# Kernel tuning notes

Measured on AMD Instinct MI355X. Metric: run time of the kernel, lower is better.

The kernel has to match this reference:

```python
import jax, jax.numpy as jnp
import numpy as np

B, S, D, H = 4, 2048, 1024, 16
DK = D // H

def setup_inputs() -> dict:
    key = jax.random.key(0)
    ks = jax.random.split(key, 13)
    std = 1.0 / np.sqrt(D)
    inp = {
        'query': jax.random.normal(ks[0], (B, S, D), jnp.float32),
        'key':   jax.random.normal(ks[1], (B, S, D), jnp.float32),
        'value': jax.random.normal(ks[2], (B, S, D), jnp.float32),
        'mask':  jax.random.randint(ks[3], (B, 1, S), 0, 2, jnp.int32),
        'Wq': jax.random.normal(ks[4], (D, D), jnp.float32) * std,
        'bq': jnp.zeros((D,), jnp.float32),
        'Wk': jax.random.normal(ks[5], (D, D), jnp.float32) * std,
        'bk': jnp.zeros((D,), jnp.float32),
        'Wv': jax.random.normal(ks[6], (D, D), jnp.float32) * std,
        'bv': jnp.zeros((D,), jnp.float32),
        'Wo': jax.random.normal(ks[7], (D, D), jnp.float32) * std,
        'bo': jnp.zeros((D,), jnp.float32),
    }
    return inp

def reference(query, key, value, mask, Wq, bq, Wk, bk, Wv, bv, Wo, bo):
    # QKV projections (torch Linear: x @ W.T + b), reshape to [B,H,S,DK]
    def proj(x, W, b):
        y = x @ W.T + b
        return y.reshape(B, S, H, DK).transpose(0, 2, 1, 3)
    q = proj(query, Wq, bq)
    k = proj(key, Wk, bk)
    v = proj(value, Wv, bv)
    scores = jnp.einsum('bhqd,bhkd->bhqk', q, k) / jnp.sqrt(jnp.float32(DK))
    # mask [B,1,S] -> unsqueeze head dim -> [B,1,1,S], broadcast over h,q
    m = mask[:, None, :, :]  # [B,1,1,S]
    scores = jnp.where(m == 0, jnp.float32(-1e9), scores)
    p = jax.nn.softmax(scores, axis=-1)  # dropout omitted (eval mode)
    x = jnp.einsum('bhqk,bhkd->bhqd', p, v)
    x = x.transpose(0, 2, 1, 3).reshape(B, S, D)
    return x @ Wo.T + bo
```

## Files before the change

kernel.cpp:

```cpp
#include <hip/hip_runtime.h>

typedef unsigned short u16;
typedef __bf16 bf16x8 __attribute__((ext_vector_type(8)));
typedef float f32x4 __attribute__((ext_vector_type(4)));
typedef u16 u16x8 __attribute__((ext_vector_type(8)));
typedef u16 u16x4 __attribute__((ext_vector_type(4)));

typedef __attribute__((address_space(1))) const unsigned char gc_u8;
typedef __attribute__((address_space(3))) unsigned char lds_u8;

__device__ inline void gload16(const void* g, void* l) {
    __builtin_amdgcn_global_load_lds((gc_u8*)g, (lds_u8*)l, 16, 0, 0);
}
__device__ inline u16 f2bf(float f) {
    union { __bf16 h; u16 u; } c; c.h = (__bf16)f; return c.u;
}
__device__ inline float bf2f(u16 u) {
    union { u16 u[2]; float f; } c; c.u[0] = 0; c.u[1] = u; return c.f;
}
__device__ inline void hard_barrier() {
    __builtin_amdgcn_sched_barrier(0);
    __builtin_amdgcn_s_barrier();
    __builtin_amdgcn_sched_barrier(0);
}
#define WAIT_LGKM0() asm volatile("s_waitcnt lgkmcnt(0)" ::: "memory")
#define WAIT_VMCNT(n) asm volatile("s_waitcnt vmcnt(" #n ")" ::: "memory")

__global__ __launch_bounds__(256) void cvt4(const float* __restrict__ s0,
                                            const float* __restrict__ s1,
                                            const float* __restrict__ s2,
                                            const float* __restrict__ s3,
                                            u16* __restrict__ d0, u16* __restrict__ d1,
                                            u16* __restrict__ d2, u16* __restrict__ d3,
                                            int n) {
    const int y = blockIdx.y;
    const float* src = (y == 0) ? s0 : (y == 1) ? s1 : (y == 2) ? s2 : s3;
    u16* dst = (y == 0) ? d0 : (y == 1) ? d1 : (y == 2) ? d2 : d3;
    int i = (blockIdx.x * 256 + threadIdx.x) * 4;
    if (i < n) {
        float4 f = *reinterpret_cast<const float4*>(src + i);
        u16x4 u = { f2bf(f.x), f2bf(f.y), f2bf(f.z), f2bf(f.w) };
        *reinterpret_cast<u16x4*>(dst + i) = u;
    }
}

__global__ __launch_bounds__(256) void gemm_qkv(const float* __restrict__ Aq,
                                                const float* __restrict__ Ak,
                                                const float* __restrict__ Av,
                                                const u16* __restrict__ Bq,
                                                const u16* __restrict__ Bk,
                                                const u16* __restrict__ Bv,
                                                const float* __restrict__ bq,
                                                const float* __restrict__ bk,
                                                const float* __restrict__ bv,
                                                u16* __restrict__ Cq,
                                                u16* __restrict__ Ck,
                                                u16* __restrict__ Cvp,
                                                int M, int N, int K) {
    __shared__ __align__(16) float Asf[2][128][32];
    __shared__ __align__(16) u16 Bs[2][128][32];
    const int z = blockIdx.z;
    const float* A = (z == 0) ? Aq : (z == 1) ? Ak : Av;
    const u16* B = (z == 0) ? Bq : (z == 1) ? Bk : Bv;
    const float* bias = (z == 0) ? bq : (z == 1) ? bk : bv;
    u16* Cv = (z == 0) ? Cq : (z == 1) ? Ck : Cvp;
    const bool vmode = (z == 2);

    const int t = threadIdx.x, lane = t & 63, w = t >> 6;
    const int wr = w >> 1, wc = w & 1;
    const int l15 = lane & 15, l16 = lane >> 4;
    const int nwg = gridDim.x, ntiles = N >> 7;
    const int wg = blockIdx.x, chunk = nwg >> 3;
    const int swz = (wg & 7) * chunk + (wg >> 3);
    const int bm = (swz / ntiles) * 128, bn = (swz % ntiles) * 128;
    const int srow = w * 16 + (lane >> 2);
    const int sgr = (lane & 3) * 8;
    const int arsub = lane >> 3;
    const int agr = ((lane & 7) ^ (lane >> 3)) * 4;
    const u16* Bb = B + (size_t)bn * K;

    f32x4 acc[4][4];
#pragma unroll
    for (int i = 0; i < 4; i++)
#pragma unroll
        for (int j = 0; j < 4; j++) acc[i][j] = (f32x4){0.f, 0.f, 0.f, 0.f};

    auto stage = [&](int c, int k0) {
#pragma unroll
        for (int ch = 0; ch < 4; ch++)
            gload16(A + (size_t)(bm + ch * 32 + w * 8 + arsub) * K + k0 + agr,
                    &Asf[c][ch * 32 + w * 8][0]);
        gload16(Bb + (size_t)srow * K + k0 + sgr,        &Bs[c][w * 16][0]);
        gload16(Bb + (size_t)(64 + srow) * K + k0 + sgr, &Bs[c][64 + w * 16][0]);
    };

    stage(0, 0);
    __syncthreads();

    const int NS = K >> 5;
    for (int i = 0; i < NS; ++i) {
        const int c = i & 1;
        WAIT_LGKM0();
        hard_barrier();
        if (i + 1 < NS) {
            stage(c ^ 1, (i + 1) * 32);
            WAIT_VMCNT(6);
        } else {
            WAIT_VMCNT(0);
        }
        hard_barrier();

        const int key = l15 & 7;
        bf16x8 afr[4], bfr[4];
#pragma unroll
        for (int mi = 0; mi < 4; mi++) {
            const int rr = wr * 64 + mi * 16 + l15;
            f32x4 lo = *(const f32x4*)&Asf[c][rr][((2 * l16) ^ key) * 4];
            f32x4 hi = *(const f32x4*)&Asf[c][rr][((2 * l16 + 1) ^ key) * 4];
            bf16x8 v;
            v[0] = (__bf16)lo[0]; v[1] = (__bf16)lo[1];
            v[2] = (__bf16)lo[2]; v[3] = (__bf16)lo[3];
            v[4] = (__bf16)hi[0]; v[5] = (__bf16)hi[1];
            v[6] = (__bf16)hi[2]; v[7] = (__bf16)hi[3];
            afr[mi] = v;
        }
#pragma unroll
        for (int ni = 0; ni < 4; ni++)
            bfr[ni] = *(const bf16x8*)&Bs[c][wc * 64 + ni * 16 + l15][l16 * 8];
#pragma unroll
        for (int mi = 0; mi < 4; mi++)
#pragma unroll
            for (int ni = 0; ni < 4; ni++)
                acc[mi][ni] = __builtin_amdgcn_mfma_f32_16x16x32_bf16(
                    afr[mi], bfr[ni], acc[mi][ni], 0, 0, 0);
    }

#pragma unroll
    for (int ni = 0; ni < 4; ni++) {
        const int col = bn + wc * 64 + ni * 16 + l15;
        const float bv2 = bias[col];
#pragma unroll
        for (int mi = 0; mi < 4; mi++) {
            const int r0 = bm + wr * 64 + mi * 16 + l16 * 4;
            if (vmode) {
                const int bb = r0 >> 11, ss = r0 & 2047;
                const int hh = col >> 6, dk = col & 63;
                u16x4 pk;
#pragma unroll
                for (int r = 0; r < 4; r++) pk[r] = f2bf(acc[mi][ni][r] + bv2);
                *(u16x4*)&Cv[(((size_t)(bb * 16 + hh) * 64 + dk) << 11) + ss] = pk;
            } else {
#pragma unroll
                for (int r = 0; r < 4; r++)
                    Cv[(size_t)(r0 + r) * N + col] = f2bf(acc[mi][ni][r] + bv2);
            }
        }
    }
}

__global__ __launch_bounds__(256) void gemm_out(const u16* __restrict__ A,
                                                const u16* __restrict__ B,
                                                const float* __restrict__ bias,
                                                float* __restrict__ Cv,
                                                int M, int N, int K) {
    __shared__ __align__(16) u16 As[2][128][32];
    __shared__ __align__(16) u16 Bs[2][128][32];
    const int t = threadIdx.x, lane = t & 63, w = t >> 6;
    const int wr = w >> 1, wc = w & 1;
    const int l15 = lane & 15, l16 = lane >> 4;
    const int nwg = gridDim.x, ntiles = N >> 7;
    const int wg = blockIdx.x, chunk = nwg >> 3;
    const int swz = (wg & 7) * chunk + (wg >> 3);
    const int bm = (swz / ntiles) * 128, bn = (swz % ntiles) * 128;
    const int srow = w * 16 + (lane >> 2);
    const int sgr = (lane & 3) * 8;
    const u16* Ab = A + (size_t)bm * K;
    const u16* Bb = B + (size_t)bn * K;

    f32x4 acc[4][4];
#pragma unroll
    for (int i = 0; i < 4; i++)
#pragma unroll
        for (int j = 0; j < 4; j++) acc[i][j] = (f32x4){0.f, 0.f, 0.f, 0.f};

    auto stage = [&](int c, int k0) {
        gload16(Ab + (size_t)srow * K + k0 + sgr,        &As[c][w * 16][0]);
        gload16(Ab + (size_t)(64 + srow) * K + k0 + sgr, &As[c][64 + w * 16][0]);
        gload16(Bb + (size_t)srow * K + k0 + sgr,        &Bs[c][w * 16][0]);
        gload16(Bb + (size_t)(64 + srow) * K + k0 + sgr, &Bs[c][64 + w * 16][0]);
    };

    stage(0, 0);
    __syncthreads();

    const int NS = K >> 5;
    for (int i = 0; i < NS; ++i) {
        const int c = i & 1;
        WAIT_LGKM0();
        hard_barrier();
        if (i + 1 < NS) {
            stage(c ^ 1, (i + 1) * 32);
            WAIT_VMCNT(4);
        } else {
            WAIT_VMCNT(0);
        }
        hard_barrier();

        bf16x8 afr[4], bfr[4];
#pragma unroll
        for (int mi = 0; mi < 4; mi++)
            afr[mi] = *(const bf16x8*)&As[c][wr * 64 + mi * 16 + l15][l16 * 8];
#pragma unroll
        for (int ni = 0; ni < 4; ni++)
            bfr[ni] = *(const bf16x8*)&Bs[c][wc * 64 + ni * 16 + l15][l16 * 8];
#pragma unroll
        for (int mi = 0; mi < 4; mi++)
#pragma unroll
            for (int ni = 0; ni < 4; ni++)
                acc[mi][ni] = __builtin_amdgcn_mfma_f32_16x16x32_bf16(
                    afr[mi], bfr[ni], acc[mi][ni], 0, 0, 0);
    }

#pragma unroll
    for (int ni = 0; ni < 4; ni++) {
        const int col = bn + wc * 64 + ni * 16 + l15;
        const float bv = bias[col];
#pragma unroll
        for (int mi = 0; mi < 4; mi++) {
            const int r0 = bm + wr * 64 + mi * 16 + l16 * 4;
#pragma unroll
            for (int r = 0; r < 4; r++)
                Cv[(size_t)(r0 + r) * N + col] = acc[mi][ni][r] + bv;
        }
    }
}

__global__ __launch_bounds__(256, 2) void attn_fwd(const u16* __restrict__ Q,
                                                   const u16* __restrict__ Kg,
                                                   const u16* __restrict__ Vt,
                                                   const int* __restrict__ mask,
                                                   u16* __restrict__ O) {
    constexpr int S = 2048, D = 1024;
    __shared__ __align__(16) u16 Kl[2][2][2][64][32];
    __shared__ __align__(16) u16 Vl[2][2][2][64][32];
    __shared__ __align__(16) u16 Pl[4][16][68];
    __shared__ unsigned Mb[64];
    const int t = threadIdx.x, lane = t & 63, w = t >> 6;
    const int l15 = lane & 15, l16 = lane >> 4;
    const int wg = blockIdx.x;
    const int swz = (wg & 7) * 64 + (wg >> 3);
    const int q0 = (swz & 7) * 256, h = (swz >> 3) & 15, b = swz >> 7;
    const int qb = q0 + w * 64;
    const int srow = w * 16 + (lane >> 2);
    const int sgr = ((lane & 3) ^ ((lane >> 3) & 3)) * 8;
    const int gsw8 = (l16 ^ ((l15 >> 1) & 3)) * 8;

    const u16* Khead = Kg + (size_t)b * S * D + h * 64;
    const u16* Vthead = Vt + (size_t)(b * 16 + h) * 64 * 2048;
    const int* mrow = mask + b * S;

    auto stage = [&](int c, int kt) {
#pragma unroll
        for (int kg = 0; kg < 2; kg++) {
            const int k0 = kt + kg * 64;
            gload16(Khead + (size_t)(k0 + srow) * D + sgr,        &Kl[c][kg][0][w * 16][0]);
            gload16(Khead + (size_t)(k0 + srow) * D + 32 + sgr,   &Kl[c][kg][1][w * 16][0]);
            gload16(Vthead + (size_t)srow * 2048 + k0 + sgr,      &Vl[c][kg][0][w * 16][0]);
            gload16(Vthead + (size_t)srow * 2048 + k0 + 32 + sgr, &Vl[c][kg][1][w * 16][0]);
        }
    };

    stage(0, 0);
#pragma unroll
    for (int j = 0; j < 8; j++) {
        unsigned long long bal = __ballot(mrow[j * 256 + w * 64 + lane] != 0);
        if (lane == 0) {
            Mb[(j * 4 + w) * 2]     = (unsigned)bal;
            Mb[(j * 4 + w) * 2 + 1] = (unsigned)(bal >> 32);
        }
    }

    constexpr float QSCALE = 0.125f * 1.44269504f;
    bf16x8 aq[4][2];
#pragma unroll
    for (int qt = 0; qt < 4; qt++)
#pragma unroll
        for (int ks = 0; ks < 2; ks++) {
            const size_t qi = ((size_t)b * S + qb + qt * 16 + l15) * D +
                              h * 64 + ks * 32 + l16 * 8;
            u16x8 raw = *(const u16x8*)&Q[qi];
            bf16x8 qv;
#pragma unroll
            for (int i = 0; i < 8; i++) qv[i] = (__bf16)(bf2f(raw[i]) * QSCALE);
            aq[qt][ks] = qv;
        }

    bf16x8 ones;
#pragma unroll
    for (int i = 0; i < 8; i++) ones[i] = (__bf16)1.0f;

    f32x4 acc[4][4];
    f32x4 accl[4];
#pragma unroll
    for (int qt = 0; qt < 4; qt++) {
        accl[qt] = (f32x4){0.f, 0.f, 0.f, 0.f};
#pragma unroll
        for (int dt = 0; dt < 4; dt++) acc[qt][dt] = (f32x4){0.f, 0.f, 0.f, 0.f};
    }

    __syncthreads();

    for (int tile = 0; tile < S / 128; ++tile) {
        const int c = tile & 1;
        const int cur = tile * 128;
        WAIT_LGKM0();
        hard_barrier();
        if (tile + 1 < S / 128) {
            stage(c ^ 1, cur + 128);
            WAIT_VMCNT(8);
        } else {
            WAIT_VMCNT(0);
        }
        hard_barrier();

#pragma unroll
        for (int kg = 0; kg < 2; kg++) {
            bf16x8 kf0[4], kf1[4], vf0[4], vf1[4];
#pragma unroll
            for (int k4 = 0; k4 < 4; k4++) {
                kf0[k4] = *(const bf16x8*)&Kl[c][kg][0][k4 * 16 + l15][gsw8];
                kf1[k4] = *(const bf16x8*)&Kl[c][kg][1][k4 * 16 + l15][gsw8];
            }
#pragma unroll
            for (int dt = 0; dt < 4; dt++) {
                vf0[dt] = *(const bf16x8*)&Vl[c][kg][0][dt * 16 + l15][gsw8];
                vf1[dt] = *(const bf16x8*)&Vl[c][kg][1][dt * 16 + l15][gsw8];
            }

            const int mb0 = (cur >> 5) + kg * 2;
            const unsigned w0 = Mb[mb0], w1 = Mb[mb0 + 1];
            float madd[4][4];
#pragma unroll
            for (int k4 = 0; k4 < 4; k4++) {
                const unsigned wsel = (k4 < 2) ? w0 : w1;
                const unsigned bits = (wsel >> ((k4 & 1) * 16 + l16 * 4)) & 0xFu;
#pragma unroll
                for (int r = 0; r < 4; r++)
                    madd[k4][r] = ((bits >> r) & 1u) ? 0.f : -1.0e9f;
            }

#pragma unroll
            for (int qt = 0; qt < 4; qt++) {
#pragma unroll
                for (int k4 = 0; k4 < 4; k4++) {
                    f32x4 z = (f32x4){0.f, 0.f, 0.f, 0.f};
                    z = __builtin_amdgcn_mfma_f32_16x16x32_bf16(kf0[k4], aq[qt][0], z, 0, 0, 0);
                    z = __builtin_amdgcn_mfma_f32_16x16x32_bf16(kf1[k4], aq[qt][1], z, 0, 0, 0);
                    u16x4 pk;
#pragma unroll
                    for (int r = 0; r < 4; r++)
                        pk[r] = f2bf(__builtin_amdgcn_exp2f(z[r] + madd[k4][r]));
                    *(u16x4*)&Pl[w][l15][k4 * 16 + l16 * 4] = pk;
                }
                bf16x8 pa0 = *(const bf16x8*)&Pl[w][l15][l16 * 8];
                bf16x8 pa1 = *(const bf16x8*)&Pl[w][l15][32 + l16 * 8];
                accl[qt] = __builtin_amdgcn_mfma_f32_16x16x32_bf16(pa0, ones, accl[qt], 0, 0, 0);
                accl[qt] = __builtin_amdgcn_mfma_f32_16x16x32_bf16(pa1, ones, accl[qt], 0, 0, 0);
#pragma unroll
                for (int dt = 0; dt < 4; dt++) {
                    acc[qt][dt] = __builtin_amdgcn_mfma_f32_16x16x32_bf16(
                        pa0, vf0[dt], acc[qt][dt], 0, 0, 0);
                    acc[qt][dt] = __builtin_amdgcn_mfma_f32_16x16x32_bf16(
                        pa1, vf1[dt], acc[qt][dt], 0, 0, 0);
                }
            }
        }
    }

#pragma unroll
    for (int qt = 0; qt < 4; qt++) {
        f32x4 inv;
#pragma unroll
        for (int r = 0; r < 4; r++) inv[r] = 1.f / accl[qt][r];
#pragma unroll
        for (int dt = 0; dt < 4; dt++)
#pragma unroll
            for (int r = 0; r < 4; r++) {
                const int tok = qb + qt * 16 + l16 * 4 + r;
                O[((size_t)b * S + tok) * D + h * 64 + dt * 16 + l15] =
                    f2bf(acc[qt][dt][r] * inv[r]);
            }
    }
}

extern "C" void kernel_launch(void* const* d_in, const int* in_sizes, int n_in,
                              void* d_out, int out_size, void* d_ws, size_t ws_size,
                              hipStream_t stream) {
    const float* query = (const float*)d_in[0];
    const float* key   = (const float*)d_in[1];
    const float* value = (const float*)d_in[2];
    const int*   mask  = (const int*)d_in[3];
    const float* Wq = (const float*)d_in[4];
    const float* bq = (const float*)d_in[5];
    const float* Wk = (const float*)d_in[6];
    const float* bk = (const float*)d_in[7];
    const float* Wv = (const float*)d_in[8];
    const float* bv = (const float*)d_in[9];
    const float* Wo = (const float*)d_in[10];
    const float* bo = (const float*)d_in[11];
    float* out = (float*)d_out;

    constexpr int S = 2048, D = 1024;
    constexpr size_t MSZ = (size_t)4 * S * D;
    constexpr size_t WSZ = (size_t)D * D;
    const size_t need = 4 * WSZ * 2 + 4 * MSZ * 2;
    if (ws_size < need) return;

    char* p = (char*)d_ws;
    u16* Wqb = (u16*)p; p += WSZ * 2;
    u16* Wkb = (u16*)p; p += WSZ * 2;
    u16* Wvb = (u16*)p; p += WSZ * 2;
    u16* Wob = (u16*)p; p += WSZ * 2;
    u16* Xb  = (u16*)p; p += MSZ * 2;
    u16* Qb  = (u16*)p; p += MSZ * 2;
    u16* Kb  = (u16*)p; p += MSZ * 2;
    u16* Vtb = (u16*)p; p += MSZ * 2;

    cvt4<<<dim3(WSZ / 1024, 4), 256, 0, stream>>>(Wq, Wk, Wv, Wo,
                                                  Wqb, Wkb, Wvb, Wob, (int)WSZ);
    gemm_qkv<<<dim3(512, 1, 3), 256, 0, stream>>>(query, key, value,
                                                  Wqb, Wkb, Wvb, bq, bk, bv,
                                                  Qb, Kb, Vtb, 8192, 1024, 1024);
    attn_fwd<<<512, 256, 0, stream>>>(Qb, Kb, Vtb, mask, Xb);
    gemm_out<<<512, 256, 0, stream>>>(Xb, Wob, bo, out, 8192, 1024, 1024);
}
```

Measured before the change: 192.1 us.

## Split attention over two key halves and combine partial sums in a second kernel

The attention kernel now splits the key dimension into two halves, launching 1024 workgroups instead of 512 so more blocks can be resident. Each block writes unnormalized bf16 partial outputs and row sums, and a new combine kernel adds the two halves and normalizes. The goal is better occupancy and load balance across the GPU. The cost is an extra kernel launch, extra global traffic for the partials, a smaller per-iteration tile, and bf16 rounding of the unnormalized partials. The output buffer is reused as scratch for the partials.

```diff
diff --git a/kernel.cpp b/kernel.cpp
--- a/kernel.cpp
+++ b/kernel.cpp
@@ -235,22 +235,26 @@
     }
 }
 
-__global__ __launch_bounds__(256, 2) void attn_fwd(const u16* __restrict__ Q,
-                                                   const u16* __restrict__ Kg,
-                                                   const u16* __restrict__ Vt,
-                                                   const int* __restrict__ mask,
-                                                   u16* __restrict__ O) {
+__global__ __launch_bounds__(256, 2) void attn_split(const u16* __restrict__ Q,
+                                                     const u16* __restrict__ Kg,
+                                                     const u16* __restrict__ Vt,
+                                                     const int* __restrict__ mask,
+                                                     u16* __restrict__ Pout,
+                                                     float* __restrict__ LS) {
     constexpr int S = 2048, D = 1024;
-    __shared__ __align__(16) u16 Kl[2][2][2][64][32];
-    __shared__ __align__(16) u16 Vl[2][2][2][64][32];
+    __shared__ __align__(16) u16 Kl[2][2][64][32];
+    __shared__ __align__(16) u16 Vl[2][2][64][32];
     __shared__ __align__(16) u16 Pl[4][16][68];
-    __shared__ unsigned Mb[64];
+    __shared__ unsigned Mb[32];
     const int t = threadIdx.x, lane = t & 63, w = t >> 6;
     const int l15 = lane & 15, l16 = lane >> 4;
     const int wg = blockIdx.x;
-    const int swz = (wg & 7) * 64 + (wg >> 3);
-    const int q0 = (swz & 7) * 256, h = (swz >> 3) & 15, b = swz >> 7;
+    const int swz = (wg & 7) * 128 + (wg >> 3);
+    const int q0 = (swz & 7) * 256;
+    const int half = (swz >> 3) & 1;
+    const int h = (swz >> 4) & 15, b = swz >> 8;
     const int qb = q0 + w * 64;
+    const int kt0 = half * 1024;
     const int srow = w * 16 + (lane >> 2);
     const int sgr = ((lane & 3) ^ ((lane >> 3) & 3)) * 8;
     const int gsw8 = (l16 ^ ((l15 >> 1) & 3)) * 8;
@@ -260,20 +264,16 @@
     const int* mrow = mask + b * S;
 
     auto stage = [&](int c, int kt) {
-#pragma unroll
-        for (int kg = 0; kg < 2; kg++) {
-            const int k0 = kt + kg * 64;
-            gload16(Khead + (size_t)(k0 + srow) * D + sgr,        &Kl[c][kg][0][w * 16][0]);
-            gload16(Khead + (size_t)(k0 + srow) * D + 32 + sgr,   &Kl[c][kg][1][w * 16][0]);
-            gload16(Vthead + (size_t)srow * 2048 + k0 + sgr,      &Vl[c][kg][0][w * 16][0]);
-            gload16(Vthead + (size_t)srow * 2048 + k0 + 32 + sgr, &Vl[c][kg][1][w * 16][0]);
-        }
+        gload16(Khead + (size_t)(kt + srow) * D + sgr,        &Kl[c][0][w * 16][0]);
+        gload16(Khead + (size_t)(kt + srow) * D + 32 + sgr,   &Kl[c][1][w * 16][0]);
+        gload16(Vthead + (size_t)srow * 2048 + kt + sgr,      &Vl[c][0][w * 16][0]);
+        gload16(Vthead + (size_t)srow * 2048 + kt + 32 + sgr, &Vl[c][1][w * 16][0]);
     };
 
-    stage(0, 0);
-#pragma unroll
-    for (int j = 0; j < 8; j++) {
-        unsigned long long bal = __ballot(mrow[j * 256 + w * 64 + lane] != 0);
+    stage(0, kt0);
+#pragma unroll
+    for (int j = 0; j < 4; j++) {
+        unsigned long long bal = __ballot(mrow[kt0 + j * 256 + w * 64 + lane] != 0);
         if (lane == 0) {
             Mb[(j * 4 + w) * 2]     = (unsigned)bal;
             Mb[(j * 4 + w) * 2 + 1] = (unsigned)(bal >> 32);
@@ -310,87 +310,105 @@
 
     __syncthreads();
 
-    for (int tile = 0; tile < S / 128; ++tile) {
+    for (int tile = 0; tile < 16; ++tile) {
         const int c = tile & 1;
-        const int cur = tile * 128;
+        const int cur = kt0 + tile * 64;
+        const int kloc = tile * 64;
         WAIT_LGKM0();
         hard_barrier();
-        if (tile + 1 < S / 128) {
-            stage(c ^ 1, cur + 128);
-            WAIT_VMCNT(8);
+        if (tile + 1 < 16) {
+            stage(c ^ 1, cur + 64);
+            WAIT_VMCNT(4);
         } else {
             WAIT_VMCNT(0);
         }
         hard_barrier();
 
-#pragma unroll
-        for (int kg = 0; kg < 2; kg++) {
-            bf16x8 kf0[4], kf1[4], vf0[4], vf1[4];
+        bf16x8 kf0[4], kf1[4], vf0[4], vf1[4];
+#pragma unroll
+        for (int k4 = 0; k4 < 4; k4++) {
+            kf0[k4] = *(const bf16x8*)&Kl[c][0][k4 * 16 + l15][gsw8];
+            kf1[k4] = *(const bf16x8*)&Kl[c][1][k4 * 16 + l15][gsw8];
+        }
+#pragma unroll
+        for (int dt = 0; dt < 4; dt++) {
+            vf0[dt] = *(const bf16x8*)&Vl[c][0][dt * 16 + l15][gsw8];
+            vf1[dt] = *(const bf16x8*)&Vl[c][1][dt * 16 + l15][gsw8];
+        }
+
+        const unsigned w0 = Mb[kloc >> 5], w1 = Mb[(kloc >> 5) + 1];
+        float madd[4][4];
+#pragma unroll
+        for (int k4 = 0; k4 < 4; k4++) {
+            const unsigned wsel = (k4 < 2) ? w0 : w1;
+            const unsigned bits = (wsel >> ((k4 & 1) * 16 + l16 * 4)) & 0xFu;
+#pragma unroll
+            for (int r = 0; r < 4; r++)
+                madd[k4][r] = ((bits >> r) & 1u) ? 0.f : -1.0e9f;
+        }
+
+#pragma unroll
+        for (int qt = 0; qt < 4; qt++) {
 #pragma unroll
             for (int k4 = 0; k4 < 4; k4++) {
-                kf0[k4] = *(const bf16x8*)&Kl[c][kg][0][k4 * 16 + l15][gsw8];
-                kf1[k4] = *(const bf16x8*)&Kl[c][kg][1][k4 * 16 + l15][gsw8];
+                f32x4 z = (f32x4){0.f, 0.f, 0.f, 0.f};
+                z = __builtin_amdgcn_mfma_f32_16x16x32_bf16(kf0[k4], aq[qt][0], z, 0, 0, 0);
+                z = __builtin_amdgcn_mfma_f32_16x16x32_bf16(kf1[k4], aq[qt][1], z, 0, 0, 0);
+                u16x4 pk;
+#pragma unroll
+                for (int r = 0; r < 4; r++)
+                    pk[r] = f2bf(__builtin_amdgcn_exp2f(z[r] + madd[k4][r]));
+                *(u16x4*)&Pl[w][l15][k4 * 16 + l16 * 4] = pk;
             }
+            bf16x8 pa0 = *(const bf16x8*)&Pl[w][l15][l16 * 8];
+            bf16x8 pa1 = *(const bf16x8*)&Pl[w][l15][32 + l16 * 8];
+            accl[qt] = __builtin_amdgcn_mfma_f32_16x16x32_bf16(pa0, ones, accl[qt], 0, 0, 0);
+            accl[qt] = __builtin_amdgcn_mfma_f32_16x16x32_bf16(pa1, ones, accl[qt], 0, 0, 0);
 #pragma unroll
             for (int dt = 0; dt < 4; dt++) {
-                vf0[dt] = *(const bf16x8*)&Vl[c][kg][0][dt * 16 + l15][gsw8];
-                vf1[dt] = *(const bf16x8*)&Vl[c][kg][1][dt * 16 + l15][gsw8];
+                acc[qt][dt] = __builtin_amdgcn_mfma_f32_16x16x32_bf16(
+                    pa0, vf0[dt], acc[qt][dt], 0, 0, 0);
+                acc[qt][dt] = __builtin_amdgcn_mfma_f32_16x16x32_bf16(
+                    pa1, vf1[dt], acc[qt][dt], 0, 0, 0);
             }
-
-            const int mb0 = (cur >> 5) + kg * 2;
-            const unsigned w0 = Mb[mb0], w1 = Mb[mb0 + 1];
-            float madd[4][4];
-#pragma unroll
-            for (int k4 = 0; k4 < 4; k4++) {
-                const unsigned wsel = (k4 < 2) ? w0 : w1;
-                const unsigned bits = (wsel >> ((k4 & 1) * 16 + l16 * 4)) & 0xFu;
-#pragma unroll
-                for (int r = 0; r < 4; r++)
-                    madd[k4][r] = ((bits >> r) & 1u) ? 0.f : -1.0e9f;
-            }
-
-#pragma unroll
-            for (int qt = 0; qt < 4; qt++) {
-#pragma unroll
-                for (int k4 = 0; k4 < 4; k4++) {
-                    f32x4 z = (f32x4){0.f, 0.f, 0.f, 0.f};
-                    z = __builtin_amdgcn_mfma_f32_16x16x32_bf16(kf0[k4], aq[qt][0], z, 0, 0, 0);
-                    z = __builtin_amdgcn_mfma_f32_16x16x32_bf16(kf1[k4], aq[qt][1], z, 0, 0, 0);
-                    u16x4 pk;
-#pragma unroll
-                    for (int r = 0; r < 4; r++)
-                        pk[r] = f2bf(__builtin_amdgcn_exp2f(z[r] + madd[k4][r]));
-                    *(u16x4*)&Pl[w][l15][k4 * 16 + l16 * 4] = pk;
-                }
-                bf16x8 pa0 = *(const bf16x8*)&Pl[w][l15][l16 * 8];
-                bf16x8 pa1 = *(const bf16x8*)&Pl[w][l15][32 + l16 * 8];
-                accl[qt] = __builtin_amdgcn_mfma_f32_16x16x32_bf16(pa0, ones, accl[qt], 0, 0, 0);
-                accl[qt] = __builtin_amdgcn_mfma_f32_16x16x32_bf16(pa1, ones, accl[qt], 0, 0, 0);
-#pragma unroll
-                for (int dt = 0; dt < 4; dt++) {
-                    acc[qt][dt] = __builtin_amdgcn_mfma_f32_16x16x32_bf16(
-                        pa0, vf0[dt], acc[qt][dt], 0, 0, 0);
-                    acc[qt][dt] = __builtin_amdgcn_mfma_f32_16x16x32_bf16(
-                        pa1, vf1[dt], acc[qt][dt], 0, 0, 0);
-                }
-            }
-        }
-    }
-
+        }
+    }
+
+    u16* Ph = Pout + (size_t)half * 8388608;
+    float* Lh = LS + (size_t)half * 131072 + (size_t)(b * 16 + h) * 2048;
 #pragma unroll
     for (int qt = 0; qt < 4; qt++) {
-        f32x4 inv;
-#pragma unroll
-        for (int r = 0; r < 4; r++) inv[r] = 1.f / accl[qt][r];
 #pragma unroll
         for (int dt = 0; dt < 4; dt++)
 #pragma unroll
             for (int r = 0; r < 4; r++) {
                 const int tok = qb + qt * 16 + l16 * 4 + r;
-                O[((size_t)b * S + tok) * D + h * 64 + dt * 16 + l15] =
-                    f2bf(acc[qt][dt][r] * inv[r]);
+                Ph[((size_t)b * S + tok) * D + h * 64 + dt * 16 + l15] =
+                    f2bf(acc[qt][dt][r]);
             }
-    }
+        if (l15 == 0)
+            *(f32x4*)&Lh[qb + qt * 16 + l16 * 4] = accl[qt];
+    }
+}
+
+__global__ __launch_bounds__(256) void attn_combine(const u16* __restrict__ Pout,
+                                                    const float* __restrict__ LS,
+                                                    u16* __restrict__ O) {
+    const size_t i = ((size_t)blockIdx.x * 256 + threadIdx.x) * 8;
+    const int tok = (int)(i >> 10);
+    const int col = (int)(i & 1023);
+    const int bb = tok >> 11, ss = tok & 2047;
+    const int hh = col >> 6;
+    const size_t li = (size_t)(bb * 16 + hh) * 2048 + ss;
+    const float l = LS[li] + LS[131072 + li];
+    const float inv = 1.f / l;
+    u16x8 a = *(const u16x8*)&Pout[i];
+    u16x8 c = *(const u16x8*)&Pout[8388608 + i];
+    u16x8 o;
+#pragma unroll
+    for (int j = 0; j < 8; j++)
+        o[j] = f2bf((bf2f(a[j]) + bf2f(c[j])) * inv);
+    *(u16x8*)&O[i] = o;
 }
 
 extern "C" void kernel_launch(void* const* d_in, const int* in_sizes, int n_in,
@@ -413,7 +431,7 @@
     constexpr int S = 2048, D = 1024;
     constexpr size_t MSZ = (size_t)4 * S * D;
     constexpr size_t WSZ = (size_t)D * D;
-    const size_t need = 4 * WSZ * 2 + 4 * MSZ * 2;
+    const size_t need = 4 * WSZ * 2 + 4 * MSZ * 2 + 2 * 131072 * 4;
     if (ws_size < need) return;
 
     char* p = (char*)d_ws;
@@ -425,12 +443,15 @@
     u16* Qb  = (u16*)p; p += MSZ * 2;
     u16* Kb  = (u16*)p; p += MSZ * 2;
     u16* Vtb = (u16*)p; p += MSZ * 2;
+    float* LS = (float*)p; p += 2 * 131072 * 4;
+    u16* Pout = (u16*)d_out;
 
     cvt4<<<dim3(WSZ / 1024, 4), 256, 0, stream>>>(Wq, Wk, Wv, Wo,
                                                   Wqb, Wkb, Wvb, Wob, (int)WSZ);
     gemm_qkv<<<dim3(512, 1, 3), 256, 0, stream>>>(query, key, value,
                                                   Wqb, Wkb, Wvb, bq, bk, bv,
                                                   Qb, Kb, Vtb, 8192, 1024, 1024);
-    attn_fwd<<<512, 256, 0, stream>>>(Qb, Kb, Vtb, mask, Xb);
+    attn_split<<<1024, 256, 0, stream>>>(Qb, Kb, Vtb, mask, Pout, LS);
+    attn_combine<<<4096, 256, 0, stream>>>(Pout, LS, Xb);
     gemm_out<<<512, 256, 0, stream>>>(Xb, Wob, bo, out, 8192, 1024, 1024);
 }
```

Measured after the change: 202.4 us. 5.4% more time.

## Fold key mask into V projection and row-sum MFMA operand instead of score bias

Applied to the files above, without the earlier changes.

Masked value rows are zeroed in the V projection epilogue, and the softmax denominator MFMA multiplies by a per-key 0/1 mask vector instead of all-ones. This removes the per-element mask bit decoding and add from the attention inner loop. The exp of masked scores is still computed but no longer contributes. With no max subtraction, masked scores that would have been pushed to -1e9 now go through exp2 unmasked, which could overflow for large scores, and a row with every key masked now gives 0/0 where the reference gives a uniform average.

```diff
diff --git a/kernel.cpp b/kernel.cpp
--- a/kernel.cpp
+++ b/kernel.cpp
@@ -53,6 +53,7 @@
                                                 const float* __restrict__ bq,
                                                 const float* __restrict__ bk,
                                                 const float* __restrict__ bv,
+                                                const int* __restrict__ Mk,
                                                 u16* __restrict__ Cq,
                                                 u16* __restrict__ Ck,
                                                 u16* __restrict__ Cvp,
@@ -145,9 +146,12 @@
             if (vmode) {
                 const int bb = r0 >> 11, ss = r0 & 2047;
                 const int hh = col >> 6, dk = col & 63;
+                const int4 m4 = *(const int4*)&Mk[bb * 2048 + ss];
                 u16x4 pk;
-#pragma unroll
-                for (int r = 0; r < 4; r++) pk[r] = f2bf(acc[mi][ni][r] + bv2);
+                pk[0] = m4.x ? f2bf(acc[mi][ni][0] + bv2) : (u16)0;
+                pk[1] = m4.y ? f2bf(acc[mi][ni][1] + bv2) : (u16)0;
+                pk[2] = m4.z ? f2bf(acc[mi][ni][2] + bv2) : (u16)0;
+                pk[3] = m4.w ? f2bf(acc[mi][ni][3] + bv2) : (u16)0;
                 *(u16x4*)&Cv[(((size_t)(bb * 16 + hh) * 64 + dk) << 11) + ss] = pk;
             } else {
 #pragma unroll
@@ -244,7 +248,7 @@
     __shared__ __align__(16) u16 Kl[2][2][2][64][32];
     __shared__ __align__(16) u16 Vl[2][2][2][64][32];
     __shared__ __align__(16) u16 Pl[4][16][68];
-    __shared__ unsigned Mb[64];
+    __shared__ __align__(16) u16 Ml[2048];
     const int t = threadIdx.x, lane = t & 63, w = t >> 6;
     const int l15 = lane & 15, l16 = lane >> 4;
     const int wg = blockIdx.x;
@@ -271,13 +275,19 @@
     };
 
     stage(0, 0);
-#pragma unroll
-    for (int j = 0; j < 8; j++) {
-        unsigned long long bal = __ballot(mrow[j * 256 + w * 64 + lane] != 0);
-        if (lane == 0) {
-            Mb[(j * 4 + w) * 2]     = (unsigned)bal;
-            Mb[(j * 4 + w) * 2 + 1] = (unsigned)(bal >> 32);
-        }
+    {
+        const int4 ia = *(const int4*)&mrow[t * 8];
+        const int4 ib = *(const int4*)&mrow[t * 8 + 4];
+        u16x8 mv;
+        mv[0] = ia.x ? (u16)0x3F80 : (u16)0;
+        mv[1] = ia.y ? (u16)0x3F80 : (u16)0;
+        mv[2] = ia.z ? (u16)0x3F80 : (u16)0;
+        mv[3] = ia.w ? (u16)0x3F80 : (u16)0;
+        mv[4] = ib.x ? (u16)0x3F80 : (u16)0;
+        mv[5] = ib.y ? (u16)0x3F80 : (u16)0;
+        mv[6] = ib.z ? (u16)0x3F80 : (u16)0;
+        mv[7] = ib.w ? (u16)0x3F80 : (u16)0;
+        *(u16x8*)&Ml[t * 8] = mv;
     }
 
     constexpr float QSCALE = 0.125f * 1.44269504f;
@@ -295,10 +305,6 @@
             aq[qt][ks] = qv;
         }
 
-    bf16x8 ones;
-#pragma unroll
-    for (int i = 0; i < 8; i++) ones[i] = (__bf16)1.0f;
-
     f32x4 acc[4][4];
     f32x4 accl[4];
 #pragma unroll
@@ -336,18 +342,9 @@
                 vf0[dt] = *(const bf16x8*)&Vl[c][kg][0][dt * 16 + l15][gsw8];
                 vf1[dt] = *(const bf16x8*)&Vl[c][kg][1][dt * 16 + l15][gsw8];
             }
-
-            const int mb0 = (cur >> 5) + kg * 2;
-            const unsigned w0 = Mb[mb0], w1 = Mb[mb0 + 1];
-            float madd[4][4];
-#pragma unroll
-            for (int k4 = 0; k4 < 4; k4++) {
-                const unsigned wsel = (k4 < 2) ? w0 : w1;
-                const unsigned bits = (wsel >> ((k4 & 1) * 16 + l16 * 4)) & 0xFu;
-#pragma unroll
-                for (int r = 0; r < 4; r++)
-                    madd[k4][r] = ((bits >> r) & 1u) ? 0.f : -1.0e9f;
-            }
+            const int kbase = cur + kg * 64;
+            bf16x8 mv0 = *(const bf16x8*)&Ml[kbase + l16 * 8];
+            bf16x8 mv1 = *(const bf16x8*)&Ml[kbase + 32 + l16 * 8];
 
 #pragma unroll
             for (int qt = 0; qt < 4; qt++) {
@@ -359,13 +356,13 @@
                     u16x4 pk;
 #pragma unroll
                     for (int r = 0; r < 4; r++)
-                        pk[r] = f2bf(__builtin_amdgcn_exp2f(z[r] + madd[k4][r]));
+                        pk[r] = f2bf(__builtin_amdgcn_exp2f(z[r]));
                     *(u16x4*)&Pl[w][l15][k4 * 16 + l16 * 4] = pk;
                 }
                 bf16x8 pa0 = *(const bf16x8*)&Pl[w][l15][l16 * 8];
                 bf16x8 pa1 = *(const bf16x8*)&Pl[w][l15][32 + l16 * 8];
-                accl[qt] = __builtin_amdgcn_mfma_f32_16x16x32_bf16(pa0, ones, accl[qt], 0, 0, 0);
-                accl[qt] = __builtin_amdgcn_mfma_f32_16x16x32_bf16(pa1, ones, accl[qt], 0, 0, 0);
+                accl[qt] = __builtin_amdgcn_mfma_f32_16x16x32_bf16(pa0, mv0, accl[qt], 0, 0, 0);
+                accl[qt] = __builtin_amdgcn_mfma_f32_16x16x32_bf16(pa1, mv1, accl[qt], 0, 0, 0);
 #pragma unroll
                 for (int dt = 0; dt < 4; dt++) {
                     acc[qt][dt] = __builtin_amdgcn_mfma_f32_16x16x32_bf16(
@@ -429,7 +426,7 @@
     cvt4<<<dim3(WSZ / 1024, 4), 256, 0, stream>>>(Wq, Wk, Wv, Wo,
                                                   Wqb, Wkb, Wvb, Wob, (int)WSZ);
     gemm_qkv<<<dim3(512, 1, 3), 256, 0, stream>>>(query, key, value,
-                                                  Wqb, Wkb, Wvb, bq, bk, bv,
+                                                  Wqb, Wkb, Wvb, bq, bk, bv, mask,
                                                   Qb, Kb, Vtb, 8192, 1024, 1024);
     attn_fwd<<<512, 256, 0, stream>>>(Qb, Kb, Vtb, mask, Xb);
     gemm_out<<<512, 256, 0, stream>>>(Xb, Wob, bo, out, 8192, 1024, 1024);
```

New measurement: 188.4 us. No clear change (-1.9%).
